# Performance work log

Measured on AMD Instinct MI355X. Metric: run time of the kernel, lower is better.

Reference implementation:

```python
import jax, jax.numpy as jnp
import numpy as np

KS = 3          # kernel_size
NH = 6          # num_heads
NUM_TOK = KS ** 3  # 27 neighbors per query


def setup_inputs() -> dict:
    key = jax.random.key(0)
    k1, k2, k3 = jax.random.split(key, 3)
    q = jax.random.normal(k1, (1, 40, 40, 40, 96), dtype=jnp.float32)
    k = jax.random.normal(k2, (1, 40, 40, 40, 96), dtype=jnp.float32)
    rpb = jax.random.normal(k3, (NH, KS, KS, KS), dtype=jnp.float32) * 0.02
    return {"q": q, "k": k, "rpb": rpb}


def _offsets():
    # torch.arange(-3//2+1, 3//2+1) == arange(-1, 2); meshgrid 'ij'; stacked -> [27, 3]
    r = jnp.arange(-1, 2, dtype=jnp.float32)
    g = jnp.stack(jnp.meshgrid(r, r, r, indexing="ij"), axis=-1)
    return g.reshape(NUM_TOK, 3)


def reference(q, k, rpb):
    B, H, W, T, C = q.shape
    hd = C // NH
    scale = hd ** -0.5
    N = H * W * T

    # queries: [B, N, nh, hd], pre-scaled
    qh = q.reshape(B, N, NH, hd) * scale

    # zero-pad keys by 1 voxel on each spatial side (matches nnf.pad on channels-first k)
    kp = jnp.pad(jnp.transpose(k, (0, 4, 1, 2, 3)),
                 ((0, 0), (0, 0), (1, 1), (1, 1), (1, 1)))

    # 27 shifted views == torch unfold over a 3x3x3 window (i slowest, matches grid order)
    wins = [kp[:, :, i:i + H, j:j + W, l:l + T]
            for i in range(KS) for j in range(KS) for l in range(KS)]
    Kw = jnp.stack(wins, axis=2)                 # [B, C, 27, H, W, T]
    Kw = Kw.reshape(B, NH, hd, NUM_TOK, N)        # [B, nh, hd, 27, N]

    # attention logits over the 27-token neighborhood
    attn = jnp.einsum("bnhd,bhdkn->bnhk", qh, Kw)  # [B, N, nh, 27]
    attn = attn + rpb.reshape(NH, NUM_TOK)[None, None, :, :]  # relative position bias
    attn = jax.nn.softmax(attn, axis=-1)

    # expected displacement: weighted sum of integer offsets -> [B, N, nh, 3]
    x = jnp.einsum("bnhk,kc->bnhc", attn, _offsets())
    x = x.reshape(B, H, W, T, NH * 3)
    return jnp.transpose(x, (0, 4, 1, 2, 3))      # [B, nh*3, H, W, T]
```

## Files before the change

### kernel.cpp

```cpp
#include <hip/hip_runtime.h>

typedef _Float16 hh2 __attribute__((ext_vector_type(2)));

#define DH 40
#define DW 40
#define DT 40
#define NC 96
#define NH 6
#define HD 16
#define NTOK 27
#define NVOX (DH * DW * DT)

#define TX 8
#define TY 4
#define TZ 8
#define HX 10
#define HY 6
#define HZ 10
#define NHALO (HX * HY * HZ)

#define TXN (DH / TX)
#define TYN (DW / TY)
#define TZN (DT / TZ)
#define NTILE (TXN * TYN * TZN)
#define NJOB (NTILE * NH)
#define NXCD 8
#define GRID 1504
#define PER_XCD (GRID / NXCD)

__device__ __forceinline__ float dot2acc(hh2 a, hh2 b, float c) {
    return __builtin_amdgcn_fdot2(a, b, c, false);
}
__device__ __forceinline__ hh2 pkrtz(float a, float b) {
    return __builtin_bit_cast(hh2, __builtin_amdgcn_cvt_pkrtz(a, b));
}

union I4H {
    int4 v[2];
    hh2 h[8];
};

__global__ __launch_bounds__(256, 8) void natt_disp_kernel(
    const float* __restrict__ q,
    const float* __restrict__ k,
    const float* __restrict__ rpb,
    float* __restrict__ out)
{
    __shared__ int4 s_k[NHALO * 2];

    const int job = (blockIdx.x & (NXCD - 1)) * PER_XCD + (blockIdx.x >> 3);
    if (job >= NJOB) return;

    const int h    = job % NH;
    const int tile = job / NH;
    const int tz = tile % TZN;
    const int ty = (tile / TZN) % TYN;
    const int tx = tile / (TZN * TYN);
    const int x0 = tx * TX, y0 = ty * TY, z0 = tz * TZ;

    const int tid = threadIdx.x;

    float rk[NTOK];
    {
        const float* rb = rpb + h * NTOK;
        #pragma unroll
        for (int kk = 0; kk < NTOK; ++kk) rk[kk] = rb[kk];
    }

    #pragma unroll
    for (int it = 0; it < 3; ++it) {
        const int n = tid + it * 256;
        if (n < NHALO) {
            const int hx = n / (HY * HZ);
            const int r  = n - hx * (HY * HZ);
            const int hy = r / HZ;
            const int hz = r - hy * HZ;
            const int gx = x0 - 1 + hx;
            const int gy = y0 - 1 + hy;
            const int gz = z0 - 1 + hz;
            I4H u;
            u.v[0] = make_int4(0, 0, 0, 0);
            u.v[1] = make_int4(0, 0, 0, 0);
            if (((unsigned)gx < DH) & ((unsigned)gy < DW) & ((unsigned)gz < DT)) {
                const float* src = k + ((size_t)((gx * DW + gy) * DT + gz)) * NC
                                     + h * HD;
                const float4 a = *(const float4*)(src);
                const float4 b = *(const float4*)(src + 4);
                const float4 c = *(const float4*)(src + 8);
                const float4 d = *(const float4*)(src + 12);
                u.h[0] = pkrtz(a.x, a.y);
                u.h[1] = pkrtz(a.z, a.w);
                u.h[2] = pkrtz(b.x, b.y);
                u.h[3] = pkrtz(b.z, b.w);
                u.h[4] = pkrtz(c.x, c.y);
                u.h[5] = pkrtz(c.z, c.w);
                u.h[6] = pkrtz(d.x, d.y);
                u.h[7] = pkrtz(d.z, d.w);
            }
            const int p = hy & 1;
            s_k[(n * 2 + 0) ^ p] = u.v[0];
            s_k[(n * 2 + 1) ^ p] = u.v[1];
        }
    }

    const int lz = tid & (TZ - 1);
    const int ly = (tid >> 3) & (TY - 1);
    const int lx = tid >> 5;
    const int vox = ((x0 + lx) * DW + (y0 + ly)) * DT + (z0 + lz);

    hh2 qh[8];
    {
        const float4* qv = (const float4*)(q + (size_t)vox * NC + h * HD);
        const float4 a = qv[0], b = qv[1], c = qv[2], d = qv[3];
        qh[0] = pkrtz(a.x, a.y);
        qh[1] = pkrtz(a.z, a.w);
        qh[2] = pkrtz(b.x, b.y);
        qh[3] = pkrtz(b.z, b.w);
        qh[4] = pkrtz(c.x, c.y);
        qh[5] = pkrtz(c.z, c.w);
        qh[6] = pkrtz(d.x, d.y);
        qh[7] = pkrtz(d.z, d.w);
    }

    __syncthreads();

    const float LOG2E = 1.44269504f;
    float sum = 0.f, sx = 0.f, sy = 0.f, sz = 0.f;

    #pragma unroll
    for (int i = 0; i < 3; ++i) {
        #pragma unroll
        for (int j = 0; j < 3; ++j) {
            const int base = ((lx + i) * HY + (ly + j)) * HZ + lz;
            const int p = (ly + j) & 1;
            #pragma unroll
            for (int ll = 0; ll < 3; ++ll) {
                const int n = base + ll;
                I4H u;
                u.v[0] = s_k[(n * 2 + 0) ^ p];
                u.v[1] = s_k[(n * 2 + 1) ^ p];
                float d = 0.0f;
                d = dot2acc(qh[0], u.h[0], d);
                d = dot2acc(qh[1], u.h[1], d);
                d = dot2acc(qh[2], u.h[2], d);
                d = dot2acc(qh[3], u.h[3], d);
                d = dot2acc(qh[4], u.h[4], d);
                d = dot2acc(qh[5], u.h[5], d);
                d = dot2acc(qh[6], u.h[6], d);
                d = dot2acc(qh[7], u.h[7], d);
                const int kk = (i * 3 + j) * 3 + ll;
                const float t = exp2f(LOG2E * fmaf(d, 0.25f, rk[kk]));
                sum += t;
                if (i == 0) sx -= t; else if (i == 2) sx += t;
                if (j == 0) sy -= t; else if (j == 2) sy += t;
                if (ll == 0) sz -= t; else if (ll == 2) sz += t;
            }
        }
    }

    const float inv = __builtin_amdgcn_rcpf(sum);

    out[((size_t)(h * 3 + 0)) * NVOX + vox] = sx * inv;
    out[((size_t)(h * 3 + 1)) * NVOX + vox] = sy * inv;
    out[((size_t)(h * 3 + 2)) * NVOX + vox] = sz * inv;
}

extern "C" void kernel_launch(void* const* d_in, const int* in_sizes, int n_in,
                              void* d_out, int out_size, void* d_ws, size_t ws_size,
                              hipStream_t stream) {
    const float* q   = (const float*)d_in[0];
    const float* k   = (const float*)d_in[1];
    const float* rpb = (const float*)d_in[2];
    float* out = (float*)d_out;

    natt_disp_kernel<<<GRID, 256, 0, stream>>>(q, k, rpb, out);
}
```

Measured before the change: 22.24 us.

## Cooperative float4-granular K and Q staging through swizzled shared memory

```diff
diff --git a/kernel.cpp b/kernel.cpp
--- a/kernel.cpp
+++ b/kernel.cpp
@@ -17,13 +17,13 @@
 #define HX 10
 #define HY 6
 #define HZ 10
-#define NHALO (HX * HY * HZ)
+#define NHALO 600
 
-#define TXN (DH / TX)
-#define TYN (DW / TY)
-#define TZN (DT / TZ)
-#define NTILE (TXN * TYN * TZN)
-#define NJOB (NTILE * NH)
+#define TXN 5
+#define TYN 10
+#define TZN 5
+#define NTILE 250
+#define NJOB 1500
 #define NXCD 8
 #define GRID 1504
 #define PER_XCD (GRID / NXCD)
@@ -31,22 +31,29 @@
 __device__ __forceinline__ float dot2acc(hh2 a, hh2 b, float c) {
     return __builtin_amdgcn_fdot2(a, b, c, false);
 }
-__device__ __forceinline__ hh2 pkrtz(float a, float b) {
-    return __builtin_bit_cast(hh2, __builtin_amdgcn_cvt_pkrtz(a, b));
+__device__ __forceinline__ unsigned int pkbits(float a, float b) {
+    return __builtin_bit_cast(unsigned int, __builtin_amdgcn_cvt_pkrtz(a, b));
+}
+__device__ __forceinline__ hh2 asz(unsigned int u) {
+    return __builtin_bit_cast(hh2, u);
+}
+__device__ __forceinline__ int swz(int C) {
+    return C ^ ((C >> 3) & 7);
 }
 
 union I4H {
-    int4 v[2];
-    hh2 h[8];
+    int4 v;
+    hh2 h[4];
 };
 
-__global__ __launch_bounds__(256, 8) void natt_disp_kernel(
+__global__ __launch_bounds__(256, 5) void natt_disp_kernel(
     const float* __restrict__ q,
     const float* __restrict__ k,
     const float* __restrict__ rpb,
     float* __restrict__ out)
 {
     __shared__ int4 s_k[NHALO * 2];
+    __shared__ int4 s_q[256 * 2];
 
     const int job = (blockIdx.x & (NXCD - 1)) * PER_XCD + (blockIdx.x >> 3);
     if (job >= NJOB) return;
@@ -67,10 +74,15 @@
         for (int kk = 0; kk < NTOK; ++kk) rk[kk] = rb[kk];
     }
 
+    const float* kh = k + h * HD;
+    const float* qh_g = q + h * HD;
+
     #pragma unroll
-    for (int it = 0; it < 3; ++it) {
-        const int n = tid + it * 256;
-        if (n < NHALO) {
+    for (int it = 0; it < 10; ++it) {
+        const int j = tid + it * 256;
+        if (j < NHALO * 4) {
+            const int n = j >> 2;
+            const int c = j & 3;
             const int hx = n / (HY * HZ);
             const int r  = n - hx * (HY * HZ);
             const int hy = r / HZ;
@@ -78,30 +90,32 @@
             const int gx = x0 - 1 + hx;
             const int gy = y0 - 1 + hy;
             const int gz = z0 - 1 + hz;
-            I4H u;
-            u.v[0] = make_int4(0, 0, 0, 0);
-            u.v[1] = make_int4(0, 0, 0, 0);
+            uint2 w; w.x = 0u; w.y = 0u;
             if (((unsigned)gx < DH) & ((unsigned)gy < DW) & ((unsigned)gz < DT)) {
-                const float* src = k + ((size_t)((gx * DW + gy) * DT + gz)) * NC
-                                     + h * HD;
-                const float4 a = *(const float4*)(src);
-                const float4 b = *(const float4*)(src + 4);
-                const float4 c = *(const float4*)(src + 8);
-                const float4 d = *(const float4*)(src + 12);
-                u.h[0] = pkrtz(a.x, a.y);
-                u.h[1] = pkrtz(a.z, a.w);
-                u.h[2] = pkrtz(b.x, b.y);
-                u.h[3] = pkrtz(b.z, b.w);
-                u.h[4] = pkrtz(c.x, c.y);
-                u.h[5] = pkrtz(c.z, c.w);
-                u.h[6] = pkrtz(d.x, d.y);
-                u.h[7] = pkrtz(d.z, d.w);
+                const float4 a = *(const float4*)(
+                    kh + ((size_t)((gx * DW + gy) * DT + gz)) * NC + c * 4);
+                w.x = pkbits(a.x, a.y);
+                w.y = pkbits(a.z, a.w);
             }
-            const int p = hy & 1;
-            s_k[(n * 2 + 0) ^ p] = u.v[0];
-            s_k[(n * 2 + 1) ^ p] = u.v[1];
+            ((uint2*)s_k)[swz(n * 2 + (c >> 1)) * 2 + (c & 1)] = w;
         }
     }
+
+    #pragma unroll
+    for (int it = 0; it < 4; ++it) {
+        const int j = tid + it * 256;
+        const int n = j >> 2;
+        const int c = j & 3;
+        const int nz = n & 7, ny = (n >> 3) & 3, nx = n >> 5;
+        const int gvox = ((x0 + nx) * DW + (y0 + ny)) * DT + (z0 + nz);
+        const float4 a = *(const float4*)(qh_g + (size_t)gvox * NC + c * 4);
+        uint2 w;
+        w.x = pkbits(a.x, a.y);
+        w.y = pkbits(a.z, a.w);
+        ((uint2*)s_q)[swz(n * 2 + (c >> 1)) * 2 + (c & 1)] = w;
+    }
+
+    __syncthreads();
 
     const int lz = tid & (TZ - 1);
     const int ly = (tid >> 3) & (TY - 1);
@@ -110,19 +124,12 @@
 
     hh2 qh[8];
     {
-        const float4* qv = (const float4*)(q + (size_t)vox * NC + h * HD);
-        const float4 a = qv[0], b = qv[1], c = qv[2], d = qv[3];
-        qh[0] = pkrtz(a.x, a.y);
-        qh[1] = pkrtz(a.z, a.w);
-        qh[2] = pkrtz(b.x, b.y);
-        qh[3] = pkrtz(b.z, b.w);
-        qh[4] = pkrtz(c.x, c.y);
-        qh[5] = pkrtz(c.z, c.w);
-        qh[6] = pkrtz(d.x, d.y);
-        qh[7] = pkrtz(d.z, d.w);
+        I4H a, b;
+        a.v = s_q[swz(tid * 2 + 0)];
+        b.v = s_q[swz(tid * 2 + 1)];
+        qh[0] = a.h[0]; qh[1] = a.h[1]; qh[2] = a.h[2]; qh[3] = a.h[3];
+        qh[4] = b.h[0]; qh[5] = b.h[1]; qh[6] = b.h[2]; qh[7] = b.h[3];
     }
-
-    __syncthreads();
 
     const float LOG2E = 1.44269504f;
     float sum = 0.f, sx = 0.f, sy = 0.f, sz = 0.f;
@@ -132,22 +139,21 @@
         #pragma unroll
         for (int j = 0; j < 3; ++j) {
             const int base = ((lx + i) * HY + (ly + j)) * HZ + lz;
-            const int p = (ly + j) & 1;
             #pragma unroll
             for (int ll = 0; ll < 3; ++ll) {
                 const int n = base + ll;
-                I4H u;
-                u.v[0] = s_k[(n * 2 + 0) ^ p];
-                u.v[1] = s_k[(n * 2 + 1) ^ p];
+                I4H u0, u1;
+                u0.v = s_k[swz(n * 2 + 0)];
+                u1.v = s_k[swz(n * 2 + 1)];
                 float d = 0.0f;
-                d = dot2acc(qh[0], u.h[0], d);
-                d = dot2acc(qh[1], u.h[1], d);
-                d = dot2acc(qh[2], u.h[2], d);
-                d = dot2acc(qh[3], u.h[3], d);
-                d = dot2acc(qh[4], u.h[4], d);
-                d = dot2acc(qh[5], u.h[5], d);
-                d = dot2acc(qh[6], u.h[6], d);
-                d = dot2acc(qh[7], u.h[7], d);
+                d = dot2acc(qh[0], u0.h[0], d);
+                d = dot2acc(qh[1], u0.h[1], d);
+                d = dot2acc(qh[2], u0.h[2], d);
+                d = dot2acc(qh[3], u0.h[3], d);
+                d = dot2acc(qh[4], u1.h[0], d);
+                d = dot2acc(qh[5], u1.h[1], d);
+                d = dot2acc(qh[6], u1.h[2], d);
+                d = dot2acc(qh[7], u1.h[3], d);
                 const int kk = (i * 3 + j) * 3 + ll;
                 const float t = exp2f(LOG2E * fmaf(d, 0.25f, rk[kk]));
                 sum += t;
```

Result: slower. 25.87 us (+16.3%).

## Enlarge tiles to 8x8x8 with 512 threads and split halo loads per quarter-head

Applied to the files above, without the earlier changes.

```diff
diff --git a/kernel.cpp b/kernel.cpp
--- a/kernel.cpp
+++ b/kernel.cpp
@@ -12,21 +12,20 @@
 #define NVOX (DH * DW * DT)
 
 #define TX 8
-#define TY 4
+#define TY 8
 #define TZ 8
 #define HX 10
-#define HY 6
+#define HY 10
 #define HZ 10
-#define NHALO (HX * HY * HZ)
+#define NHALO 1000
 
-#define TXN (DH / TX)
-#define TYN (DW / TY)
-#define TZN (DT / TZ)
-#define NTILE (TXN * TYN * TZN)
-#define NJOB (NTILE * NH)
-#define NXCD 8
-#define GRID 1504
-#define PER_XCD (GRID / NXCD)
+#define TXN 5
+#define TYN 5
+#define TZN 5
+#define NTILE 125
+#define NJOB 750
+#define GRID 752
+#define PER_XCD 94
 
 __device__ __forceinline__ float dot2acc(hh2 a, hh2 b, float c) {
     return __builtin_amdgcn_fdot2(a, b, c, false);
@@ -34,13 +33,16 @@
 __device__ __forceinline__ hh2 pkrtz(float a, float b) {
     return __builtin_bit_cast(hh2, __builtin_amdgcn_cvt_pkrtz(a, b));
 }
+__device__ __forceinline__ unsigned int pkbits(float a, float b) {
+    return __builtin_bit_cast(unsigned int, __builtin_amdgcn_cvt_pkrtz(a, b));
+}
 
 union I4H {
     int4 v[2];
     hh2 h[8];
 };
 
-__global__ __launch_bounds__(256, 8) void natt_disp_kernel(
+__global__ __launch_bounds__(512, 4) void natt_disp_kernel(
     const float* __restrict__ q,
     const float* __restrict__ k,
     const float* __restrict__ rpb,
@@ -48,7 +50,7 @@
 {
     __shared__ int4 s_k[NHALO * 2];
 
-    const int job = (blockIdx.x & (NXCD - 1)) * PER_XCD + (blockIdx.x >> 3);
+    const int job = (blockIdx.x & 7) * PER_XCD + (blockIdx.x >> 3);
     if (job >= NJOB) return;
 
     const int h    = job % NH;
@@ -67,10 +69,14 @@
         for (int kk = 0; kk < NTOK; ++kk) rk[kk] = rb[kk];
     }
 
+    const float* kh = k + h * HD;
+
     #pragma unroll
-    for (int it = 0; it < 3; ++it) {
-        const int n = tid + it * 256;
-        if (n < NHALO) {
+    for (int it = 0; it < 8; ++it) {
+        const int jj = tid + it * 512;
+        if (jj < NHALO * 4) {
+            const int n = jj >> 2;
+            const int c = jj & 3;
             const int hx = n / (HY * HZ);
             const int r  = n - hx * (HY * HZ);
             const int hy = r / HZ;
@@ -78,34 +84,21 @@
             const int gx = x0 - 1 + hx;
             const int gy = y0 - 1 + hy;
             const int gz = z0 - 1 + hz;
-            I4H u;
-            u.v[0] = make_int4(0, 0, 0, 0);
-            u.v[1] = make_int4(0, 0, 0, 0);
+            uint2 w; w.x = 0u; w.y = 0u;
             if (((unsigned)gx < DH) & ((unsigned)gy < DW) & ((unsigned)gz < DT)) {
-                const float* src = k + ((size_t)((gx * DW + gy) * DT + gz)) * NC
-                                     + h * HD;
-                const float4 a = *(const float4*)(src);
-                const float4 b = *(const float4*)(src + 4);
-                const float4 c = *(const float4*)(src + 8);
-                const float4 d = *(const float4*)(src + 12);
-                u.h[0] = pkrtz(a.x, a.y);
-                u.h[1] = pkrtz(a.z, a.w);
-                u.h[2] = pkrtz(b.x, b.y);
-                u.h[3] = pkrtz(b.z, b.w);
-                u.h[4] = pkrtz(c.x, c.y);
-                u.h[5] = pkrtz(c.z, c.w);
-                u.h[6] = pkrtz(d.x, d.y);
-                u.h[7] = pkrtz(d.z, d.w);
+                const float4 a = *(const float4*)(
+                    kh + ((size_t)((gx * DW + gy) * DT + gz)) * NC + c * 4);
+                w.x = pkbits(a.x, a.y);
+                w.y = pkbits(a.z, a.w);
             }
             const int p = hy & 1;
-            s_k[(n * 2 + 0) ^ p] = u.v[0];
-            s_k[(n * 2 + 1) ^ p] = u.v[1];
+            ((uint2*)s_k)[((n * 2 + (c >> 1)) ^ p) * 2 + (c & 1)] = w;
         }
     }
 
-    const int lz = tid & (TZ - 1);
-    const int ly = (tid >> 3) & (TY - 1);
-    const int lx = tid >> 5;
+    const int lz = tid & 7;
+    const int ly = (tid >> 3) & 7;
+    const int lx = tid >> 6;
     const int vox = ((x0 + lx) * DW + (y0 + ly)) * DT + (z0 + lz);
 
     hh2 qh[8];
@@ -124,6 +117,7 @@
 
     __syncthreads();
 
+    const float SC2 = 0.36067376f;
     const float LOG2E = 1.44269504f;
     float sum = 0.f, sx = 0.f, sy = 0.f, sz = 0.f;
 
@@ -149,7 +143,7 @@
                 d = dot2acc(qh[6], u.h[6], d);
                 d = dot2acc(qh[7], u.h[7], d);
                 const int kk = (i * 3 + j) * 3 + ll;
-                const float t = exp2f(LOG2E * fmaf(d, 0.25f, rk[kk]));
+                const float t = exp2f(fmaf(d, SC2, rk[kk] * LOG2E));
                 sum += t;
                 if (i == 0) sx -= t; else if (i == 2) sx += t;
                 if (j == 0) sy -= t; else if (j == 2) sy += t;
@@ -173,5 +167,5 @@
     const float* rpb = (const float*)d_in[2];
     float* out = (float*)d_out;
 
-    natt_disp_kernel<<<GRID, 256, 0, stream>>>(q, k, rpb, out);
+    natt_disp_kernel<<<GRID, 512, 0, stream>>>(q, k, rpb, out);
 }
```

Measured after the change: 20.28 us (median of 2 runs). 8.8% less time.
